# Kernel optimization log

Hardware: AMD Instinct MI355X
Metric: run time of the kernel (lower is better)

## Reference

```python
import jax, jax.numpy as jnp
import numpy as np


def setup_inputs() -> dict:
    key = jax.random.key(0)
    k1, k2, k3, k4 = jax.random.split(key, 4)
    B, S, D, R = 8, 1024, 1024, 256
    batch = jax.random.normal(k1, (B, S, D), dtype=jnp.float32)
    proj_L = jax.random.uniform(k2, (D, R), dtype=jnp.float32, minval=-0.05, maxval=0.05)
    proj_R = jax.random.uniform(k3, (R, D), dtype=jnp.float32, minval=-0.05, maxval=0.05)
    bias = jax.random.uniform(k4, (1,), dtype=jnp.float32, minval=-0.05, maxval=0.05)
    return {"batch": batch, "proj_L": proj_L, "proj_R": proj_R, "bias": bias}


def reference(batch, proj_L, proj_R, bias):
    # logits[b,i,j] = h_i^T (L @ R) h_j + bias
    # Efficient factored form (same math, avoids O(B*S^2*D) intermediates):
    # left[b,i,r] = (batch @ L)[b,i,r]; right[b,j,r] = (batch @ R^T)[b,j,r]
    left = jnp.einsum('bid,dr->bir', batch, proj_L)    # (B,S,R)
    right = jnp.einsum('bjd,rd->bjr', batch, proj_R)   # (B,S,R)
    logits = jnp.einsum('bir,bjr->bij', left, right) + bias[0]
    return logits
```

## Files before the change

kernel.cpp:

```cpp
#include <hip/hip_runtime.h>

typedef __bf16 bf16_t;
typedef __bf16 bf16x8 __attribute__((ext_vector_type(8)));
typedef __bf16 bf16x4 __attribute__((ext_vector_type(4)));
typedef float f32x4 __attribute__((ext_vector_type(4)));

__device__ __forceinline__ void async16(const void* g, void* l) {
  __builtin_amdgcn_global_load_lds(
      (const __attribute__((address_space(1))) unsigned int*)g,
      (__attribute__((address_space(3))) unsigned int*)l,
      16, 0, 0);
}

__global__ void prep_Bcat(const float* __restrict__ projL,
                          const float* __restrict__ projR,
                          bf16_t* __restrict__ Bcat) {
  const int t = threadIdx.x;
  if (blockIdx.x < 256) {
    int i = blockIdx.x * 256 + t;
    float4 v = ((const float4*)projR)[i];
    bf16x4 o;
    o[0] = (bf16_t)v.x; o[1] = (bf16_t)v.y; o[2] = (bf16_t)v.z; o[3] = (bf16_t)v.w;
    ((bf16x4*)(Bcat + (long)256 * 1024))[i] = o;
  } else {
    __shared__ float tile[32][33];
    const int bb = blockIdx.x - 256;
    const int n0 = (bb & 7) * 32;
    const int k0 = (bb >> 3) * 32;
    const int tx = t & 31;
    const int ty = t >> 5;
#pragma unroll
    for (int i = 0; i < 32; i += 8)
      tile[ty + i][tx] = projL[(long)(k0 + ty + i) * 256 + n0 + tx];
    __syncthreads();
#pragma unroll
    for (int i = 0; i < 32; i += 8)
      Bcat[(long)(n0 + ty + i) * 1024 + k0 + tx] = (bf16_t)tile[tx][ty + i];
  }
}

__global__ __launch_bounds__(256, 2) void gemm1_fusedA(
    const float* __restrict__ batch, const bf16_t* __restrict__ Bcat,
    bf16_t* __restrict__ LR) {
  const int bx = blockIdx.x;
  const int tm = (bx & 127) * 64;
  const int tn = (bx >> 7) * 128;

  __shared__ __attribute__((aligned(16))) bf16_t As[4 * 2048];
  __shared__ __attribute__((aligned(16))) bf16_t Bs[4 * 4096];

  const int t = threadIdx.x;
  const int lane = t & 63;
  const int quad = lane >> 4;
  const int l15 = lane & 15;
  const int wave = t >> 6;
  const int wr = (wave >> 1) * 32;
  const int wc = (wave & 1) * 64;

  const int rS = t >> 2;
  const int cS = (t & 3) * 8;
  const bf16_t* gB = Bcat + (long)(tn + rS) * 1024 + cS;
  bf16_t* lB = Bs + t * 8;

  const int rA = t >> 4;
  const int cA = (t & 15) * 8;
  const float* gA = batch + (long)(tm + rA) * 1024 + cA;
  bf16_t* lA = As + (cA >> 5) * 2048 + (cA & 31);

  f32x4 acc[2][4];
#pragma unroll
  for (int i = 0; i < 2; ++i)
#pragma unroll
    for (int j = 0; j < 4; ++j)
      acc[i][j] = (f32x4){0.f, 0.f, 0.f, 0.f};

  for (int s = 0; s < 8; ++s) {
    const int k0 = s * 128;
    float4 fa[4], fb[4];
#pragma unroll
    for (int i = 0; i < 4; ++i) {
      const float* p = gA + k0 + (long)16 * i * 1024;
      fa[i] = *(const float4*)p;
      fb[i] = *(const float4*)(p + 4);
    }
#pragma unroll
    for (int kc = 0; kc < 4; ++kc) {
      async16(gB + k0 + kc * 32, lB + kc * 4096);
      async16(gB + k0 + kc * 32 + (long)64 * 1024, lB + kc * 4096 + 2048);
    }
#pragma unroll
    for (int i = 0; i < 4; ++i) {
      bf16x8 v;
      v[0] = (bf16_t)fa[i].x; v[1] = (bf16_t)fa[i].y;
      v[2] = (bf16_t)fa[i].z; v[3] = (bf16_t)fa[i].w;
      v[4] = (bf16_t)fb[i].x; v[5] = (bf16_t)fb[i].y;
      v[6] = (bf16_t)fb[i].z; v[7] = (bf16_t)fb[i].w;
      *(bf16x8*)(lA + (rA + 16 * i) * 32) = v;
    }
    __syncthreads();

#pragma unroll
    for (int kc = 0; kc < 4; ++kc) {
      const bf16_t* Ak = As + kc * 2048;
      const bf16_t* Bk = Bs + kc * 4096;
      bf16x8 af[2], bv[4];
#pragma unroll
      for (int i = 0; i < 2; ++i)
        af[i] = *(const bf16x8*)(Ak + (wr + i * 16 + l15) * 32 + quad * 8);
#pragma unroll
      for (int j = 0; j < 4; ++j)
        bv[j] = *(const bf16x8*)(Bk + (wc + j * 16 + l15) * 32 + quad * 8);
#pragma unroll
      for (int i = 0; i < 2; ++i)
#pragma unroll
        for (int j = 0; j < 4; ++j)
          acc[i][j] = __builtin_amdgcn_mfma_f32_16x16x32_bf16(af[i], bv[j],
                                                              acc[i][j], 0, 0, 0);
    }
    __syncthreads();
  }

#pragma unroll
  for (int i = 0; i < 2; ++i) {
    const int r0 = tm + wr + i * 16 + quad * 4;
#pragma unroll
    for (int j = 0; j < 4; ++j) {
      const int c0 = tn + wc + j * 16 + l15;
#pragma unroll
      for (int r = 0; r < 4; ++r)
        LR[(long)(r0 + r) * 512 + c0] = (bf16_t)acc[i][j][r];
    }
  }
}

__global__ __launch_bounds__(256) void gemm2(const bf16_t* __restrict__ LR,
                                             float* __restrict__ out,
                                             const float* __restrict__ bias) {
  const int bx = blockIdx.x;
  const int bz = bx & 7;
  const int tile = bx >> 3;
  const int tm = (tile & 7) * 128;
  const int tn = (tile >> 3) * 128;
  const bf16_t* LRb = LR + (long)bz * 1024 * 512;

  __shared__ __attribute__((aligned(16))) bf16_t As[4 * 4096];
  __shared__ __attribute__((aligned(16))) bf16_t Bs[4 * 4096];

  const int t = threadIdx.x;
  const int lane = t & 63;
  const int quad = lane >> 4;
  const int l15 = lane & 15;
  const int wave = t >> 6;
  const int wr = (wave >> 1) * 64;
  const int wc = (wave & 1) * 64;

  const int rS = t >> 2;
  const int cS = (t & 3) * 8;
  const bf16_t* gA = LRb + (long)(tm + rS) * 512 + cS;
  const bf16_t* gB = LRb + (long)(tn + rS) * 512 + 256 + cS;
  bf16_t* lA = As + t * 8;
  bf16_t* lB = Bs + t * 8;

  f32x4 acc[4][4];
#pragma unroll
  for (int i = 0; i < 4; ++i)
#pragma unroll
    for (int j = 0; j < 4; ++j)
      acc[i][j] = (f32x4){0.f, 0.f, 0.f, 0.f};

#pragma unroll
  for (int s = 0; s < 2; ++s) {
    const int k0 = s * 128;
#pragma unroll
    for (int kc = 0; kc < 4; ++kc) {
      const int ko = k0 + kc * 32;
      async16(gA + ko, lA + kc * 4096);
      async16(gA + ko + (long)64 * 512, lA + kc * 4096 + 2048);
      async16(gB + ko, lB + kc * 4096);
      async16(gB + ko + (long)64 * 512, lB + kc * 4096 + 2048);
    }
    __syncthreads();

#pragma unroll
    for (int kc = 0; kc < 4; ++kc) {
      const bf16_t* Ak = As + kc * 4096;
      const bf16_t* Bk = Bs + kc * 4096;
      bf16x8 af[4], bv[4];
#pragma unroll
      for (int i = 0; i < 4; ++i)
        af[i] = *(const bf16x8*)(Ak + (wr + i * 16 + l15) * 32 + quad * 8);
#pragma unroll
      for (int j = 0; j < 4; ++j)
        bv[j] = *(const bf16x8*)(Bk + (wc + j * 16 + l15) * 32 + quad * 8);
#pragma unroll
      for (int i = 0; i < 4; ++i)
#pragma unroll
        for (int j = 0; j < 4; ++j)
          acc[i][j] = __builtin_amdgcn_mfma_f32_16x16x32_bf16(af[i], bv[j],
                                                              acc[i][j], 0, 0, 0);
    }
    __syncthreads();
  }

  float* C = out + (long)bz * 1024 * 1024;
  const float bvadd = bias[0];
#pragma unroll
  for (int i = 0; i < 4; ++i) {
    const int r0 = tm + wr + i * 16 + quad * 4;
#pragma unroll
    for (int j = 0; j < 4; ++j) {
      const int c0 = tn + wc + j * 16 + l15;
#pragma unroll
      for (int r = 0; r < 4; ++r)
        C[(long)(r0 + r) * 1024 + c0] = acc[i][j][r] + bvadd;
    }
  }
}

extern "C" void kernel_launch(void* const* d_in, const int* in_sizes, int n_in,
                              void* d_out, int out_size, void* d_ws,
                              size_t ws_size, hipStream_t stream) {
  const float* batch = (const float*)d_in[0];
  const float* projL = (const float*)d_in[1];
  const float* projR = (const float*)d_in[2];
  const float* bias = (const float*)d_in[3];
  float* out = (float*)d_out;

  char* ws = (char*)d_ws;
  bf16_t* Bcat = (bf16_t*)ws;
  bf16_t* LR = (bf16_t*)(ws + (long)512 * 1024 * 2);

  prep_Bcat<<<512, 256, 0, stream>>>(projL, projR, Bcat);

  gemm1_fusedA<<<512, 256, 0, stream>>>(batch, Bcat, LR);

  gemm2<<<512, 256, 0, stream>>>(LR, out, bias);
}
```

Before: 111.5 us.

## Prefetch next A tile in gemm1 and double-buffer LDS stages in gemm2

In gemm1, the fp32 loads of the next K-slice of the batch now start right after the barrier, so they overlap the current slice's MFMA work. gemm2 switches from two 128-wide K stages to four 64-wide stages. It uses two LDS buffers, issuing async loads for the next stage while computing on the current one, and adds a launch bound of 2 blocks per CU. This is meant to hide global-load latency behind compute. The cost is more live registers in gemm1 and more barrier steps in gemm2.

Result: no change. 110.1 us (-1.3%).

```diff
diff --git a/kernel.cpp b/kernel.cpp
--- a/kernel.cpp
+++ b/kernel.cpp
@@ -74,15 +74,16 @@
     for (int j = 0; j < 4; ++j)
       acc[i][j] = (f32x4){0.f, 0.f, 0.f, 0.f};
 
+  float4 fa[4], fb[4];
+#pragma unroll
+  for (int i = 0; i < 4; ++i) {
+    const float* p = gA + (long)16 * i * 1024;
+    fa[i] = *(const float4*)p;
+    fb[i] = *(const float4*)(p + 4);
+  }
+
   for (int s = 0; s < 8; ++s) {
     const int k0 = s * 128;
-    float4 fa[4], fb[4];
-#pragma unroll
-    for (int i = 0; i < 4; ++i) {
-      const float* p = gA + k0 + (long)16 * i * 1024;
-      fa[i] = *(const float4*)p;
-      fb[i] = *(const float4*)(p + 4);
-    }
 #pragma unroll
     for (int kc = 0; kc < 4; ++kc) {
       async16(gB + k0 + kc * 32, lB + kc * 4096);
@@ -99,6 +100,15 @@
     }
     __syncthreads();
 
+    if (s < 7) {
+#pragma unroll
+      for (int i = 0; i < 4; ++i) {
+        const float* p = gA + (s + 1) * 128 + (long)16 * i * 1024;
+        fa[i] = *(const float4*)p;
+        fb[i] = *(const float4*)(p + 4);
+      }
+    }
+
 #pragma unroll
     for (int kc = 0; kc < 4; ++kc) {
       const bf16_t* Ak = As + kc * 2048;
@@ -133,9 +143,9 @@
   }
 }
 
-__global__ __launch_bounds__(256) void gemm2(const bf16_t* __restrict__ LR,
-                                             float* __restrict__ out,
-                                             const float* __restrict__ bias) {
+__global__ __launch_bounds__(256, 2) void gemm2(const bf16_t* __restrict__ LR,
+                                                float* __restrict__ out,
+                                                const float* __restrict__ bias) {
   const int bx = blockIdx.x;
   const int bz = bx & 7;
   const int tile = bx >> 3;
@@ -143,8 +153,8 @@
   const int tn = (tile >> 3) * 128;
   const bf16_t* LRb = LR + (long)bz * 1024 * 512;
 
-  __shared__ __attribute__((aligned(16))) bf16_t As[4 * 4096];
-  __shared__ __attribute__((aligned(16))) bf16_t Bs[4 * 4096];
+  __shared__ __attribute__((aligned(16))) bf16_t As[2 * 8192];
+  __shared__ __attribute__((aligned(16))) bf16_t Bs[2 * 8192];
 
   const int t = threadIdx.x;
   const int lane = t & 63;
@@ -158,8 +168,6 @@
   const int cS = (t & 3) * 8;
   const bf16_t* gA = LRb + (long)(tm + rS) * 512 + cS;
   const bf16_t* gB = LRb + (long)(tn + rS) * 512 + 256 + cS;
-  bf16_t* lA = As + t * 8;
-  bf16_t* lB = Bs + t * 8;
 
   f32x4 acc[4][4];
 #pragma unroll
@@ -168,23 +176,32 @@
     for (int j = 0; j < 4; ++j)
       acc[i][j] = (f32x4){0.f, 0.f, 0.f, 0.f};
 
-#pragma unroll
-  for (int s = 0; s < 2; ++s) {
-    const int k0 = s * 128;
-#pragma unroll
-    for (int kc = 0; kc < 4; ++kc) {
+  auto STAGE = [&](int buf, int s) {
+    const int k0 = s * 64;
+    bf16_t* dA = As + buf * 8192 + t * 8;
+    bf16_t* dB = Bs + buf * 8192 + t * 8;
+#pragma unroll
+    for (int kc = 0; kc < 2; ++kc) {
       const int ko = k0 + kc * 32;
-      async16(gA + ko, lA + kc * 4096);
-      async16(gA + ko + (long)64 * 512, lA + kc * 4096 + 2048);
-      async16(gB + ko, lB + kc * 4096);
-      async16(gB + ko + (long)64 * 512, lB + kc * 4096 + 2048);
-    }
-    __syncthreads();
-
-#pragma unroll
-    for (int kc = 0; kc < 4; ++kc) {
-      const bf16_t* Ak = As + kc * 4096;
-      const bf16_t* Bk = Bs + kc * 4096;
+      async16(gA + ko, dA + kc * 4096);
+      async16(gA + ko + (long)64 * 512, dA + kc * 4096 + 2048);
+      async16(gB + ko, dB + kc * 4096);
+      async16(gB + ko + (long)64 * 512, dB + kc * 4096 + 2048);
+    }
+  };
+
+  STAGE(0, 0);
+  __syncthreads();
+
+#pragma unroll
+  for (int s = 0; s < 4; ++s) {
+    if (s < 3) STAGE((s + 1) & 1, s + 1);
+    const bf16_t* Ab = As + (s & 1) * 8192;
+    const bf16_t* Bb = Bs + (s & 1) * 8192;
+#pragma unroll
+    for (int kc = 0; kc < 2; ++kc) {
+      const bf16_t* Ak = Ab + kc * 4096;
+      const bf16_t* Bk = Bb + kc * 4096;
       bf16x8 af[4], bv[4];
 #pragma unroll
       for (int i = 0; i < 4; ++i)
@@ -199,7 +216,7 @@
           acc[i][j] = __builtin_amdgcn_mfma_f32_16x16x32_bf16(af[i], bv[j],
                                                               acc[i][j], 0, 0, 0);
     }
-    __syncthreads();
+    if (s < 3) __syncthreads();
   }
 
   float* C = out + (long)bz * 1024 * 1024;
```
